# Kernel tuning notes

Measured on AMD Instinct MI355X. Metric: run time of the kernel, lower is better.

## Reference

```python
import jax, jax.numpy as jnp
import numpy as np

B, S, NH, NKV, D = 2, 2048, 32, 8, 128

def setup_inputs() -> dict:
    key = jax.random.key(0)
    kq, kk, kv = jax.random.split(key, 3)
    query = jax.random.normal(kq, (B, S, NH, D), dtype=jnp.float32)
    k_ = jax.random.normal(kk, (B, S, NKV, D), dtype=jnp.float32)
    v_ = jax.random.normal(kv, (B, S, NKV, D), dtype=jnp.float32)
    # causal additive mask, broadcastable to [B, NH, S, S]
    causal = jnp.tril(jnp.ones((S, S), dtype=bool))
    attn_mask = jnp.where(causal, 0.0, -1e9).astype(jnp.float32)[None, None]
    return {"query": query, "key": k_, "value": v_, "attn_mask": attn_mask}

def reference(query, key, value, attn_mask):
    nh, nkv = query.shape[-2], key.shape[-2]
    # [B, S, H, D] -> [B, H, S, D]
    q = jnp.swapaxes(query, -3, -2)
    k = jnp.swapaxes(key, -3, -2)
    v = jnpp_swap(value) if False else jnp.swapaxes(value, -3, -2)
    qpk = nh // nkv
    if qpk > 1:
        k = jnp.repeat(k, qpk, axis=-3)
        v = jnp.repeat(v, qpk, axis=-3)
    scale = q.shape[-1] ** (-0.5)
    # [B, H, Sq, Sk]
    score = jnp.einsum('bhqd,bhkd->bhqk', q, k) * scale
    score = score + attn_mask
    probs = jax.nn.softmax(score.astype(jnp.float32), axis=-1).astype(q.dtype)
    out = jnp.einsum('bhqk,bhkd->bhqd', probs, v)
    # [B, H, S, D] -> [B, S, H, D]
    return jnp.swapaxes(out, 1, 2)
```

## Files before the change

kernel.cpp:

```cpp
#include <hip/hip_runtime.h>
#include <hip/hip_bf16.h>

#define B_    2
#define S_    2048
#define NH_   32
#define NKV_  8
#define D_    128
#define QBLK  128
#define KVBLK 64

#define KVH_STRIDE 524288u
#define V_WS_OFF   8388608u

typedef __bf16 bf16x8 __attribute__((ext_vector_type(8)));
typedef float  f32x16 __attribute__((ext_vector_type(16)));
typedef unsigned short u16x4 __attribute__((ext_vector_type(4)));
typedef unsigned int   u32x4 __attribute__((ext_vector_type(4)));

typedef const __attribute__((address_space(1))) void* gptr_t;
typedef __attribute__((address_space(3))) void*       lptr_t;

__device__ inline unsigned short f2bfu(float f) {
    unsigned u = __builtin_bit_cast(unsigned, f);
    u += 0x7fffu + ((u >> 16) & 1u);
    return (unsigned short)(u >> 16);
}
__device__ inline __bf16 f2bf(float f) {
    unsigned short s = f2bfu(f);
    return __builtin_bit_cast(__bf16, s);
}
__device__ inline unsigned packbf(float lo, float hi) {
    return (unsigned)f2bfu(lo) | ((unsigned)f2bfu(hi) << 16);
}

__device__ inline void* kaddr(unsigned short* base, int row, int byteInRow) {
    return (void*)((char*)base + row * 256 + (byteInRow ^ ((row & 7) << 4)));
}
__device__ inline void* vaddr(unsigned short* base, int row, int byteInRow) {
    return (void*)((char*)base + row * 128 + (byteInRow ^ ((row & 7) << 4)));
}

__global__ __launch_bounds__(256)
void convert_k(const float* __restrict__ kin, unsigned short* __restrict__ kout) {
    const int g = blockIdx.x * 256 + threadIdx.x;
    const size_t o = (size_t)g * 4;
    const int d   = (int)(o & 127);
    const int k   = (int)((o >> 7) & 2047);
    const int kvh = (int)((o >> 18) & 7);
    const int b   = (int)(o >> 21);
    const float* src = kin + (((size_t)(b * 2048 + k)) * 8 + kvh) * 128 + d;
    float4 x = *reinterpret_cast<const float4*>(src);
    u16x4 u = { f2bfu(x.x), f2bfu(x.y), f2bfu(x.z), f2bfu(x.w) };
    *reinterpret_cast<u16x4*>(kout + o) = u;
}

__global__ __launch_bounds__(256)
void convert_v(const float* __restrict__ vin, unsigned short* __restrict__ vout) {
    __shared__ unsigned short vl[64][136];
    const int t  = threadIdx.x;
    const int bb = blockIdx.x;
    const int j  = bb & 31;
    const int bk = bb >> 5;
    const int b  = bk >> 3, kvh = bk & 7;
    const float* base = vin + (((size_t)(b * 2048 + j * 64)) * 8 + kvh) * 128;
    #pragma unroll
    for (int i = 0; i < 8; ++i) {
        const int row = i * 8 + (t >> 5), c4 = t & 31;
        float4 x = *reinterpret_cast<const float4*>(base + (size_t)row * 1024 + c4 * 4);
        u16x4 u = { f2bfu(x.x), f2bfu(x.y), f2bfu(x.z), f2bfu(x.w) };
        *reinterpret_cast<u16x4*>(&vl[row][c4 * 4]) = u;
    }
    __syncthreads();
    unsigned short* out = vout + (size_t)bb * 8192;
    #pragma unroll
    for (int it = 0; it < 4; ++it) {
        const int c = it * 256 + t;
        const int d = c >> 3, k0 = (c & 7) * 8;
        u16x4 lo = { vl[k0 + 0][d], vl[k0 + 1][d], vl[k0 + 2][d], vl[k0 + 3][d] };
        u16x4 hi = { vl[k0 + 4][d], vl[k0 + 5][d], vl[k0 + 6][d], vl[k0 + 7][d] };
        *reinterpret_cast<u16x4*>(out + (size_t)d * 64 + k0)     = lo;
        *reinterpret_cast<u16x4*>(out + (size_t)d * 64 + k0 + 4) = hi;
    }
}

__global__ __launch_bounds__(256, 3)
void sdpa_fwd(const float* __restrict__ qg, const unsigned short* __restrict__ kws,
              const unsigned short* __restrict__ vws, float* __restrict__ og)
{
    __shared__ __align__(16) unsigned short Kb[2][8192];
    __shared__ __align__(16) unsigned short Vb[8192];

    const int bx  = blockIdx.x;
    const int qt  = 15 - (bx >> 6);
    const int r   = bx & 63;
    const int kvh = r & 7;
    const int h   = kvh * 4 + ((r >> 3) & 3);
    const int b   = (r >> 5) & 1;
    const int bk  = b * 8 + kvh;

    const int t   = threadIdx.x;
    const int w   = t >> 6;
    const int l   = t & 63;
    const int l32 = l & 31;
    const int lh  = l >> 5;

    const float scale = 0.08838834764831845f;
    const int qmin_w = qt * QBLK + w * 32;
    const int qgl    = qmin_w + l32;

    const int koff = ((t >> 4) << 8) + ((((t & 15) << 4)) ^ (((t >> 4) & 7) << 4));
    const int voff = ((t >> 3) << 7) + ((((t & 7) << 4)) ^ (((t >> 3) & 7) << 4));
    const char* Khead = (const char*)kws + (size_t)bk * KVH_STRIDE;
    const char* Vhead = (const char*)vws + (size_t)bk * KVH_STRIDE;

    bf16x8 qf[8];
    {
        const float* Qp = qg + (((size_t)b * S_ + qgl) * NH_ + h) * D_;
        #pragma unroll
        for (int dc = 0; dc < 8; ++dc) {
            const int d0 = dc * 16 + lh * 8;
            float4 a = *reinterpret_cast<const float4*>(Qp + d0);
            float4 c = *reinterpret_cast<const float4*>(Qp + d0 + 4);
            bf16x8 f;
            f[0] = f2bf(a.x * scale); f[1] = f2bf(a.y * scale);
            f[2] = f2bf(a.z * scale); f[3] = f2bf(a.w * scale);
            f[4] = f2bf(c.x * scale); f[5] = f2bf(c.y * scale);
            f[6] = f2bf(c.z * scale); f[7] = f2bf(c.w * scale);
            qf[dc] = f;
        }
    }

    f32x16 acc[4] = {};
    float mrow = -INFINITY, lrow = 0.0f;

    auto issueK = [&](int j, int c) {
        const char* ks = Khead + (size_t)j * 16384 + koff;
        char* kl = (char*)&Kb[c][0] + t * 16;
        #pragma unroll
        for (int i = 0; i < 4; ++i)
            __builtin_amdgcn_global_load_lds((gptr_t)(ks + i * 4096),
                                             (lptr_t)(kl + i * 4096), 16, 0, 0);
    };
    auto issueV = [&](int j) {
        const char* vs = Vhead + (size_t)j * 16384 + voff;
        char* vl = (char*)&Vb[0] + t * 16;
        #pragma unroll
        for (int i = 0; i < 4; ++i)
            __builtin_amdgcn_global_load_lds((gptr_t)(vs + i * 4096),
                                             (lptr_t)(vl + i * 4096), 16, 0, 0);
    };

    issueK(0, 0);
    const int jmax = 2 * qt + 1;

    for (int j = 0; j <= jmax; ++j) {
        const int cur = j & 1;
        const int jbase = j * KVBLK;
        const bool live = (jbase <= qmin_w + 31);

        __builtin_amdgcn_s_barrier();
        __builtin_amdgcn_sched_barrier(0);
        issueV(j);
        if (j < jmax) {
            issueK(j + 1, cur ^ 1);
            asm volatile("s_waitcnt vmcnt(8)" ::: "memory");
        } else {
            asm volatile("s_waitcnt vmcnt(4)" ::: "memory");
        }
        __builtin_amdgcn_s_barrier();
        __builtin_amdgcn_sched_barrier(0);

        f32x16 sc0 = {}, sc1 = {};
        bf16x8 pa[4];
        if (live) {
            unsigned short* kbuf = &Kb[cur][0];
            __builtin_amdgcn_s_setprio(1);
            #pragma unroll
            for (int dc = 0; dc < 8; ++dc) {
                bf16x8 kf0 = *reinterpret_cast<const bf16x8*>(
                    kaddr(kbuf, l32, dc * 32 + lh * 16));
                sc0 = __builtin_amdgcn_mfma_f32_32x32x16_bf16(kf0, qf[dc], sc0, 0, 0, 0);
                bf16x8 kf1 = *reinterpret_cast<const bf16x8*>(
                    kaddr(kbuf, 32 + l32, dc * 32 + lh * 16));
                sc1 = __builtin_amdgcn_mfma_f32_32x32x16_bf16(kf1, qf[dc], sc1, 0, 0, 0);
            }
            __builtin_amdgcn_s_setprio(0);

            if (jbase + (KVBLK - 1) > qmin_w) {
                #pragma unroll
                for (int rr = 0; rr < 16; ++rr) {
                    const int kk = jbase + (rr & 3) + 8 * (rr >> 2) + 4 * lh;
                    if (kk > qgl)      sc0[rr] = -INFINITY;
                    if (kk + 32 > qgl) sc1[rr] = -INFINITY;
                }
            }

            float mt = -INFINITY;
            #pragma unroll
            for (int rr = 0; rr < 16; ++rr) mt = fmaxf(mt, fmaxf(sc0[rr], sc1[rr]));
            mt = fmaxf(mt, __shfl_xor(mt, 32));
            const float mnew = fmaxf(mrow, mt);
            if (!__all(mnew - mrow <= 8.0f)) {
                const float resc = __expf(mrow - mnew);
                lrow *= resc;
                #pragma unroll
                for (int dt = 0; dt < 4; ++dt) acc[dt] *= resc;
                mrow = mnew;
            }
            float ps = 0.0f;
            #pragma unroll
            for (int rr = 0; rr < 16; ++rr) {
                sc0[rr] = __expf(sc0[rr] - mrow);
                sc1[rr] = __expf(sc1[rr] - mrow);
                ps += sc0[rr] + sc1[rr];
            }
            ps += __shfl_xor(ps, 32);
            lrow += ps;

            #pragma unroll
            for (int g = 0; g < 4; ++g) {
                float p0, p1, p2, p3, p4, p5, p6, p7;
                if (g == 0) { p0=sc0[0]; p1=sc0[1]; p2=sc0[2]; p3=sc0[3];
                              p4=sc0[4]; p5=sc0[5]; p6=sc0[6]; p7=sc0[7]; }
                else if (g == 1) { p0=sc0[8];  p1=sc0[9];  p2=sc0[10]; p3=sc0[11];
                                   p4=sc0[12]; p5=sc0[13]; p6=sc0[14]; p7=sc0[15]; }
                else if (g == 2) { p0=sc1[0]; p1=sc1[1]; p2=sc1[2]; p3=sc1[3];
                                   p4=sc1[4]; p5=sc1[5]; p6=sc1[6]; p7=sc1[7]; }
                else { p0=sc1[8];  p1=sc1[9];  p2=sc1[10]; p3=sc1[11];
                       p4=sc1[12]; p5=sc1[13]; p6=sc1[14]; p7=sc1[15]; }
                unsigned a0 = packbf(p0, p1), b0 = packbf(p4, p5);
                unsigned a1 = packbf(p2, p3), b1 = packbf(p6, p7);
                auto s02 = __builtin_amdgcn_permlane32_swap((int)a0, (int)b0, false, false);
                auto s13 = __builtin_amdgcn_permlane32_swap((int)a1, (int)b1, false, false);
                u32x4 dw = { (unsigned)s02[0], (unsigned)s13[0],
                             (unsigned)s02[1], (unsigned)s13[1] };
                pa[g] = __builtin_bit_cast(bf16x8, dw);
            }
        }

        if (j < jmax) asm volatile("s_waitcnt vmcnt(4)" ::: "memory");
        else          asm volatile("s_waitcnt vmcnt(0)" ::: "memory");
        __builtin_amdgcn_s_barrier();
        __builtin_amdgcn_sched_barrier(0);

        if (live) {
            __builtin_amdgcn_s_setprio(1);
            #pragma unroll
            for (int kc = 0; kc < 4; ++kc) {
                #pragma unroll
                for (int dt = 0; dt < 4; ++dt) {
                    bf16x8 vf = *reinterpret_cast<const bf16x8*>(
                        vaddr(&Vb[0], dt * 32 + l32, kc * 32 + lh * 16));
                    acc[dt] = __builtin_amdgcn_mfma_f32_32x32x16_bf16(vf, pa[kc], acc[dt], 0, 0, 0);
                }
            }
            __builtin_amdgcn_s_setprio(0);
        }
    }

    const float invl = 1.0f / lrow;
    float* Op = og + (((size_t)b * S_ + qgl) * NH_ + h) * D_;
    #pragma unroll
    for (int dt = 0; dt < 4; ++dt) {
        #pragma unroll
        for (int rg = 0; rg < 4; ++rg) {
            float4 st;
            st.x = acc[dt][rg * 4 + 0] * invl;
            st.y = acc[dt][rg * 4 + 1] * invl;
            st.z = acc[dt][rg * 4 + 2] * invl;
            st.w = acc[dt][rg * 4 + 3] * invl;
            *reinterpret_cast<float4*>(Op + dt * 32 + rg * 8 + lh * 4) = st;
        }
    }
}

extern "C" void kernel_launch(void* const* d_in, const int* in_sizes, int n_in,
                              void* d_out, int out_size, void* d_ws, size_t ws_size,
                              hipStream_t stream) {
    const float* q = (const float*)d_in[0];
    const float* k = (const float*)d_in[1];
    const float* v = (const float*)d_in[2];
    float* out = (float*)d_out;
    unsigned short* kws = (unsigned short*)d_ws;
    unsigned short* vws = (unsigned short*)((char*)d_ws + V_WS_OFF);

    convert_k<<<dim3(4096), 256, 0, stream>>>(k, kws);
    convert_v<<<dim3(512),  256, 0, stream>>>(v, vws);
    sdpa_fwd <<<dim3(1024), 256, 0, stream>>>(q, kws, vws, out);
}
```

Measured before the change: 122.2 us.

## Double-buffer V tiles, use exp2 softmax, and tree-reduce row max/sum

V is now double-buffered alongside K and prefetched one tile ahead, which removes the mid-iteration wait and barrier between the QK and PV phases. The cost is more LDS (occupancy hint lowered from 3 to 2 blocks per CU). The log2(e) factor is folded into the Q scale so softmax can use the native exp2 instruction, and the rescale threshold is widened to match. Row max and sum reductions become tree-shaped to shorten dependency chains, and bf16 conversion uses the compiler's native cast instead of manual rounding.

```diff
diff --git a/kernel.cpp b/kernel.cpp
--- a/kernel.cpp
+++ b/kernel.cpp
@@ -20,17 +20,17 @@
 typedef const __attribute__((address_space(1))) void* gptr_t;
 typedef __attribute__((address_space(3))) void*       lptr_t;
 
-__device__ inline unsigned short f2bfu(float f) {
-    unsigned u = __builtin_bit_cast(unsigned, f);
-    u += 0x7fffu + ((u >> 16) & 1u);
-    return (unsigned short)(u >> 16);
-}
-__device__ inline __bf16 f2bf(float f) {
-    unsigned short s = f2bfu(f);
-    return __builtin_bit_cast(__bf16, s);
+#if __has_builtin(__builtin_amdgcn_exp2f)
+#define EXP2(x) __builtin_amdgcn_exp2f(x)
+#else
+#define EXP2(x) exp2f(x)
+#endif
+
+__device__ inline unsigned short bfu(float f) {
+    return __builtin_bit_cast(unsigned short, (__bf16)f);
 }
 __device__ inline unsigned packbf(float lo, float hi) {
-    return (unsigned)f2bfu(lo) | ((unsigned)f2bfu(hi) << 16);
+    return (unsigned)bfu(lo) | ((unsigned)bfu(hi) << 16);
 }
 
 __device__ inline void* kaddr(unsigned short* base, int row, int byteInRow) {
@@ -50,7 +50,7 @@
     const int b   = (int)(o >> 21);
     const float* src = kin + (((size_t)(b * 2048 + k)) * 8 + kvh) * 128 + d;
     float4 x = *reinterpret_cast<const float4*>(src);
-    u16x4 u = { f2bfu(x.x), f2bfu(x.y), f2bfu(x.z), f2bfu(x.w) };
+    u16x4 u = { bfu(x.x), bfu(x.y), bfu(x.z), bfu(x.w) };
     *reinterpret_cast<u16x4*>(kout + o) = u;
 }
 
@@ -67,7 +67,7 @@
     for (int i = 0; i < 8; ++i) {
         const int row = i * 8 + (t >> 5), c4 = t & 31;
         float4 x = *reinterpret_cast<const float4*>(base + (size_t)row * 1024 + c4 * 4);
-        u16x4 u = { f2bfu(x.x), f2bfu(x.y), f2bfu(x.z), f2bfu(x.w) };
+        u16x4 u = { bfu(x.x), bfu(x.y), bfu(x.z), bfu(x.w) };
         *reinterpret_cast<u16x4*>(&vl[row][c4 * 4]) = u;
     }
     __syncthreads();
@@ -83,12 +83,12 @@
     }
 }
 
-__global__ __launch_bounds__(256, 3)
+__global__ __launch_bounds__(256, 2)
 void sdpa_fwd(const float* __restrict__ qg, const unsigned short* __restrict__ kws,
               const unsigned short* __restrict__ vws, float* __restrict__ og)
 {
     __shared__ __align__(16) unsigned short Kb[2][8192];
-    __shared__ __align__(16) unsigned short Vb[8192];
+    __shared__ __align__(16) unsigned short Vb[2][8192];
 
     const int bx  = blockIdx.x;
     const int qt  = 15 - (bx >> 6);
@@ -104,7 +104,7 @@
     const int l32 = l & 31;
     const int lh  = l >> 5;
 
-    const float scale = 0.08838834764831845f;
+    const float scale = 0.08838834764831845f * 1.4426950408889634f;
     const int qmin_w = qt * QBLK + w * 32;
     const int qgl    = qmin_w + l32;
 
@@ -122,10 +122,10 @@
             float4 a = *reinterpret_cast<const float4*>(Qp + d0);
             float4 c = *reinterpret_cast<const float4*>(Qp + d0 + 4);
             bf16x8 f;
-            f[0] = f2bf(a.x * scale); f[1] = f2bf(a.y * scale);
-            f[2] = f2bf(a.z * scale); f[3] = f2bf(a.w * scale);
-            f[4] = f2bf(c.x * scale); f[5] = f2bf(c.y * scale);
-            f[6] = f2bf(c.z * scale); f[7] = f2bf(c.w * scale);
+            f[0] = (__bf16)(a.x * scale); f[1] = (__bf16)(a.y * scale);
+            f[2] = (__bf16)(a.z * scale); f[3] = (__bf16)(a.w * scale);
+            f[4] = (__bf16)(c.x * scale); f[5] = (__bf16)(c.y * scale);
+            f[6] = (__bf16)(c.z * scale); f[7] = (__bf16)(c.w * scale);
             qf[dc] = f;
         }
     }
@@ -141,16 +141,16 @@
             __builtin_amdgcn_global_load_lds((gptr_t)(ks + i * 4096),
                                              (lptr_t)(kl + i * 4096), 16, 0, 0);
     };
-    auto issueV = [&](int j) {
+    auto issueV = [&](int j, int c) {
         const char* vs = Vhead + (size_t)j * 16384 + voff;
-        char* vl = (char*)&Vb[0] + t * 16;
+        char* vl = (char*)&Vb[c][0] + t * 16;
         #pragma unroll
         for (int i = 0; i < 4; ++i)
             __builtin_amdgcn_global_load_lds((gptr_t)(vs + i * 4096),
                                              (lptr_t)(vl + i * 4096), 16, 0, 0);
     };
 
-    issueK(0, 0);
+    issueV(0, 0); issueK(0, 0);
     const int jmax = 2 * qt + 1;
 
     for (int j = 0; j <= jmax; ++j) {
@@ -160,20 +160,21 @@
 
         __builtin_amdgcn_s_barrier();
         __builtin_amdgcn_sched_barrier(0);
-        issueV(j);
         if (j < jmax) {
+            issueV(j + 1, cur ^ 1);
             issueK(j + 1, cur ^ 1);
             asm volatile("s_waitcnt vmcnt(8)" ::: "memory");
         } else {
-            asm volatile("s_waitcnt vmcnt(4)" ::: "memory");
+            asm volatile("s_waitcnt vmcnt(0)" ::: "memory");
         }
         __builtin_amdgcn_s_barrier();
         __builtin_amdgcn_sched_barrier(0);
 
-        f32x16 sc0 = {}, sc1 = {};
-        bf16x8 pa[4];
         if (live) {
             unsigned short* kbuf = &Kb[cur][0];
+            unsigned short* vbuf = &Vb[cur][0];
+
+            f32x16 sc0 = {}, sc1 = {};
             __builtin_amdgcn_s_setprio(1);
             #pragma unroll
             for (int dc = 0; dc < 8; ++dc) {
@@ -195,28 +196,39 @@
                 }
             }
 
-            float mt = -INFINITY;
-            #pragma unroll
-            for (int rr = 0; rr < 16; ++rr) mt = fmaxf(mt, fmaxf(sc0[rr], sc1[rr]));
-            mt = fmaxf(mt, __shfl_xor(mt, 32));
+            float mx[16];
+            #pragma unroll
+            for (int rr = 0; rr < 16; ++rr) mx[rr] = fmaxf(sc0[rr], sc1[rr]);
+            #pragma unroll
+            for (int s = 8; s > 0; s >>= 1)
+                #pragma unroll
+                for (int i = 0; i < 8; ++i)
+                    if (i < s) mx[i] = fmaxf(mx[i], mx[i + s]);
+            float mt = fmaxf(mx[0], __shfl_xor(mx[0], 32));
             const float mnew = fmaxf(mrow, mt);
-            if (!__all(mnew - mrow <= 8.0f)) {
-                const float resc = __expf(mrow - mnew);
+            if (!__all(mnew - mrow <= 11.5f)) {
+                const float resc = EXP2(mrow - mnew);
                 lrow *= resc;
                 #pragma unroll
                 for (int dt = 0; dt < 4; ++dt) acc[dt] *= resc;
                 mrow = mnew;
             }
-            float ps = 0.0f;
             #pragma unroll
             for (int rr = 0; rr < 16; ++rr) {
-                sc0[rr] = __expf(sc0[rr] - mrow);
-                sc1[rr] = __expf(sc1[rr] - mrow);
-                ps += sc0[rr] + sc1[rr];
-            }
-            ps += __shfl_xor(ps, 32);
-            lrow += ps;
-
+                sc0[rr] = EXP2(sc0[rr] - mrow);
+                sc1[rr] = EXP2(sc1[rr] - mrow);
+            }
+            float sm[16];
+            #pragma unroll
+            for (int rr = 0; rr < 16; ++rr) sm[rr] = sc0[rr] + sc1[rr];
+            #pragma unroll
+            for (int s = 8; s > 0; s >>= 1)
+                #pragma unroll
+                for (int i = 0; i < 8; ++i)
+                    if (i < s) sm[i] += sm[i + s];
+            lrow += sm[0] + __shfl_xor(sm[0], 32);
+
+            bf16x8 pa[4];
             #pragma unroll
             for (int g = 0; g < 4; ++g) {
                 float p0, p1, p2, p3, p4, p5, p6, p7;
@@ -236,21 +248,14 @@
                              (unsigned)s02[1], (unsigned)s13[1] };
                 pa[g] = __builtin_bit_cast(bf16x8, dw);
             }
-        }
-
-        if (j < jmax) asm volatile("s_waitcnt vmcnt(4)" ::: "memory");
-        else          asm volatile("s_waitcnt vmcnt(0)" ::: "memory");
-        __builtin_amdgcn_s_barrier();
-        __builtin_amdgcn_sched_barrier(0);
-
-        if (live) {
+
             __builtin_amdgcn_s_setprio(1);
             #pragma unroll
             for (int kc = 0; kc < 4; ++kc) {
                 #pragma unroll
                 for (int dt = 0; dt < 4; ++dt) {
                     bf16x8 vf = *reinterpret_cast<const bf16x8*>(
-                        vaddr(&Vb[0], dt * 32 + l32, kc * 32 + lh * 16));
+                        vaddr(vbuf, dt * 32 + l32, kc * 32 + lh * 16));
                     acc[dt] = __builtin_amdgcn_mfma_f32_32x32x16_bf16(vf, pa[kc], acc[dt], 0, 0, 0);
                 }
             }
```

Result: faster. 115.2 us (-5.7%).
